# Optimization experiments

Hardware: AMD Instinct MI355X
Metric: run time of the kernel (lower is better)

Reference implementation:

```python
import jax, jax.numpy as jnp
import numpy as np

IN_DIM = 4
H_DIM = 128
OBS_LEN = 15
PRED_LEN = 15
BATCH = 32768


def _lstm_cell(x, h, c, Wih, Whh, bih, bhh):
    # PyTorch gate order: i, f, g, o
    gates = x @ Wih.T + h @ Whh.T + (bih + bhh)  # [B, 4H]
    i, f, g, o = jnp.split(gates, 4, axis=-1)
    c_new = jax.nn.sigmoid(f) * c + jax.nn.sigmoid(i) * jnp.tanh(g)
    h_new = jax.nn.sigmoid(o) * jnp.tanh(c_new)
    return h_new, c_new


def setup_inputs() -> dict:
    key = jax.random.key(0)
    ks = jax.random.split(key, 12)
    s = 1.0 / np.sqrt(H_DIM)  # PyTorch LSTM/Linear uniform init bound
    u = lambda k, shape: jax.random.uniform(k, shape, jnp.float32, -s, s)
    return {
        "x": jax.random.normal(ks[0], (BATCH, OBS_LEN, IN_DIM), jnp.float32),
        "enc_Wih": u(ks[1], (4 * H_DIM, IN_DIM)),
        "enc_Whh": u(ks[2], (4 * H_DIM, H_DIM)),
        "enc_bih": u(ks[3], (4 * H_DIM,)),
        "enc_bhh": u(ks[4], (4 * H_DIM,)),
        "dec_Wih": u(ks[5], (4 * H_DIM, IN_DIM)),
        "dec_Whh": u(ks[6], (4 * H_DIM, H_DIM)),
        "dec_bih": u(ks[7], (4 * H_DIM,)),
        "dec_bhh": u(ks[8], (4 * H_DIM,)),
        "out_W": u(ks[9], (IN_DIM, H_DIM)),
        "out_b": u(ks[10], (IN_DIM,)),
    }


def reference(x, enc_Wih, enc_Whh, enc_bih, enc_bhh,
              dec_Wih, dec_Whh, dec_bih, dec_bhh, out_W, out_b):
    B = x.shape[0]
    h0 = jnp.zeros((B, H_DIM), x.dtype)
    c0 = jnp.zeros((B, H_DIM), x.dtype)

    # ---- encode: run LSTM over time, keep final h ----
    def enc_step(carry, xt):
        h, c = carry
        h, c = _lstm_cell(xt, h, c, enc_Wih, enc_Whh, enc_bih, enc_bhh)
        return (h, c), None

    (h_enc, _), _ = jax.lax.scan(enc_step, (h0, c0), jnp.swapaxes(x, 0, 1))

    def dec_step(carry, _):
        x0, h, c = carry
        h, c = _lstm_cell(x0, h, c, dec_Wih, dec_Whh, dec_bih, dec_bhh)
        x0 = h @ out_W.T + out_b  # [B, IN_DIM]
        return (x0, h, c), x0

    x0 = x[:, -1, :]
    _, preds = jax.lax.scan(dec_step, (x0, h_enc, h_enc), None, length=PRED_LEN)
    return jnp.swapaxes(preds, 0, 1)  # [B, PRED_LEN, IN_DIM]
```

## Files before the change

### kernel.cpp

```cpp
#include <hip/hip_runtime.h>

#define HD   128
#define SEQ  15
#define BN   32
#define LDH  168
#define KT   5
#define NTHR 512

typedef __bf16 bf16x8 __attribute__((ext_vector_type(8)));
typedef unsigned short us8 __attribute__((ext_vector_type(8)));
typedef float f32x4 __attribute__((ext_vector_type(4)));

__device__ __forceinline__ unsigned short f2bf(float f) {
  unsigned int u = __builtin_bit_cast(unsigned int, f);
  u += 0x7fffu + ((u >> 16) & 1u);
  return (unsigned short)(u >> 16);
}
__device__ __forceinline__ float bfl(unsigned int u) {
  return __builtin_bit_cast(float, u << 16);
}
__device__ __forceinline__ float bfh(unsigned int u) {
  return __builtin_bit_cast(float, u & 0xffff0000u);
}
__device__ __forceinline__ float sigm(float v) {
  return __builtin_amdgcn_rcpf(1.0f + __expf(-v));
}
__device__ __forceinline__ float tanh_(float v) {
  return 1.0f - 2.0f * __builtin_amdgcn_rcpf(1.0f + __expf(2.0f * v));
}

__global__ __launch_bounds__(NTHR, 2) void lstm_encdec_kernel(
    const float* __restrict__ x,
    const float* __restrict__ eWih, const float* __restrict__ eWhh,
    const float* __restrict__ ebih, const float* __restrict__ ebhh,
    const float* __restrict__ dWih, const float* __restrict__ dWhh,
    const float* __restrict__ dbih, const float* __restrict__ dbhh,
    const float* __restrict__ oW,  const float* __restrict__ ob,
    float* __restrict__ out)
{
  const int tid  = (int)threadIdx.x;
  const int wv   = tid >> 6;
  const int lane = tid & 63;
  const int l15  = lane & 15;
  const int lk   = lane >> 4;
  const int b0   = (int)blockIdx.x * BN;

  __shared__ alignas(16) unsigned short hbuf[BN][LDH];
  __shared__ float ow_l[4][132];
  __shared__ float ob_l[4];

  bf16x8 bw[4][KT];
  float  bias[4];
  f32x4  cst[2], hst[2];

  for (int i = tid; i < BN * LDH; i += NTHR) ((unsigned short*)hbuf)[i] = 0;

  #pragma unroll
  for (int m = 0; m < 2; ++m)
    #pragma unroll
    for (int j = 0; j < 4; ++j) { cst[m][j] = 0.0f; hst[m][j] = 0.0f; }

  auto load_w = [&](const float* Wih, const float* Whh,
                    const float* bih, const float* bhh, bool fold) {
    #pragma unroll
    for (int g = 0; g < 4; ++g) {
      const int gc = g * HD + wv * 16 + l15;
      float wi[4];
      #pragma unroll
      for (int d = 0; d < 4; ++d) wi[d] = Wih[gc * 4 + d];
      #pragma unroll
      for (int kt = 0; kt < KT; ++kt) {
        const int k0 = kt * 32 + lk * 8;
        float v[8];
        if (k0 < HD) {
          const float4* p = (const float4*)&Whh[(size_t)gc * HD + k0];
          const float4 u0 = p[0], u1 = p[1];
          v[0]=u0.x; v[1]=u0.y; v[2]=u0.z; v[3]=u0.w;
          v[4]=u1.x; v[5]=u1.y; v[6]=u1.z; v[7]=u1.w;
          if (fold) {
            #pragma unroll
            for (int j = 0; j < 8; ++j) {
              float s = v[j];
              #pragma unroll
              for (int d = 0; d < 4; ++d) s += wi[d] * oW[d * HD + k0 + j];
              v[j] = s;
            }
          }
        } else {
          #pragma unroll
          for (int j = 0; j < 8; ++j) {
            v[j] = 0.0f;
            if (j < 4 && lk == 0) v[j] = wi[j];
          }
        }
        us8 u;
        #pragma unroll
        for (int j = 0; j < 8; ++j) u[j] = f2bf(v[j]);
        bw[g][kt] = __builtin_bit_cast(bf16x8, u);
      }
      float bb = bih[gc] + bhh[gc];
      if (fold) {
        #pragma unroll
        for (int d = 0; d < 4; ++d) bb += ob[d] * Wih[gc * 4 + d];
      }
      bias[g] = bb;
    }
  };

  auto mfma_step = [&](f32x4 (&acc)[2][4]) {
    #pragma unroll
    for (int m = 0; m < 2; ++m)
      #pragma unroll
      for (int g = 0; g < 4; ++g)
        #pragma unroll
        for (int j = 0; j < 4; ++j) acc[m][g][j] = bias[g];
    #pragma unroll
    for (int kt = 0; kt < KT; ++kt) {
      #pragma unroll
      for (int m = 0; m < 2; ++m) {
        const bf16x8 a = __builtin_bit_cast(bf16x8,
            *(const uint4*)&hbuf[m * 16 + l15][kt * 32 + lk * 8]);
        #pragma unroll
        for (int g = 0; g < 4; ++g)
          acc[m][g] = __builtin_amdgcn_mfma_f32_16x16x32_bf16(a, bw[g][kt], acc[m][g], 0, 0, 0);
      }
    }
  };

  auto act_update = [&](f32x4 (&acc)[2][4]) {
    #pragma unroll
    for (int m = 0; m < 2; ++m) {
      #pragma unroll
      for (int j = 0; j < 4; ++j) {
        const float iv = sigm(acc[m][0][j]);
        const float fv = sigm(acc[m][1][j]);
        const float gv = tanh_(acc[m][2][j]);
        const float ov = sigm(acc[m][3][j]);
        const float cv = fv * cst[m][j] + iv * gv;
        cst[m][j] = cv;
        hst[m][j] = ov * tanh_(cv);
      }
    }
  };

  auto write_h = [&]() {
    #pragma unroll
    for (int m = 0; m < 2; ++m)
      #pragma unroll
      for (int j = 0; j < 4; ++j)
        hbuf[m * 16 + lk * 4 + j][wv * 16 + l15] = f2bf(hst[m][j]);
  };

  auto proj = [&](int b, int d) {
    float s = ob_l[d];
    #pragma unroll
    for (int k = 0; k < HD; k += 8) {
      const uint4 hv = *(const uint4*)&hbuf[b][k];
      const float* wr = &ow_l[d][k];
      s += bfl(hv.x) * wr[0] + bfh(hv.x) * wr[1]
         + bfl(hv.y) * wr[2] + bfh(hv.y) * wr[3]
         + bfl(hv.z) * wr[4] + bfh(hv.z) * wr[5]
         + bfl(hv.w) * wr[6] + bfh(hv.w) * wr[7];
    }
    return s;
  };

  load_w(eWih, eWhh, ebih, ebhh, false);
  __syncthreads();
  if (tid < BN) {
    const float4 xv = *(const float4*)&x[(size_t)(b0 + tid) * 60];
    *(unsigned int*)&hbuf[tid][HD]     = (unsigned)f2bf(xv.x) | ((unsigned)f2bf(xv.y) << 16);
    *(unsigned int*)&hbuf[tid][HD + 2] = (unsigned)f2bf(xv.z) | ((unsigned)f2bf(xv.w) << 16);
  }
  __syncthreads();

  for (int t = 0; t < SEQ; ++t) {
    f32x4 acc[2][4];
    mfma_step(acc);
    __syncthreads();
    act_update(acc);
    write_h();
    if (t < SEQ - 1 && tid < BN) {
      const float4 xv = *(const float4*)&x[(size_t)(b0 + tid) * 60 + (t + 1) * 4];
      *(unsigned int*)&hbuf[tid][HD]     = (unsigned)f2bf(xv.x) | ((unsigned)f2bf(xv.y) << 16);
      *(unsigned int*)&hbuf[tid][HD + 2] = (unsigned)f2bf(xv.z) | ((unsigned)f2bf(xv.w) << 16);
    }
    __syncthreads();
  }

  cst[0] = hst[0]; cst[1] = hst[1];
  load_w(dWih, dWhh, dbih, dbhh, true);
  for (int i = tid; i < 4 * HD; i += NTHR) ow_l[i >> 7][i & 127] = oW[i];
  if (tid < 4) ob_l[tid] = ob[tid];
  __syncthreads();
  if (tid < 128) {
    const int b = tid >> 2, d = tid & 3;
    const float x0v = proj(b, d);
    const float x14 = x[(size_t)(b0 + b) * 60 + 56 + d];
    hbuf[b][HD + d] = f2bf(x14 - x0v);
  }
  __syncthreads();

  for (int t = 0; t < SEQ; ++t) {
    f32x4 acc[2][4];
    mfma_step(acc);
    __syncthreads();
    act_update(acc);
    write_h();
    if (t == 0 && tid < BN) {
      *(unsigned int*)&hbuf[tid][HD]     = 0u;
      *(unsigned int*)&hbuf[tid][HD + 2] = 0u;
    }
    __syncthreads();
    if (tid < 128) {
      const int b = tid >> 2, d = tid & 3;
      out[(size_t)(b0 + b) * 60 + t * 4 + d] = proj(b, d);
    }
  }
}

extern "C" void kernel_launch(void* const* d_in, const int* in_sizes, int n_in,
                              void* d_out, int out_size, void* d_ws, size_t ws_size,
                              hipStream_t stream) {
  const float* x    = (const float*)d_in[0];
  const float* eWih = (const float*)d_in[1];
  const float* eWhh = (const float*)d_in[2];
  const float* ebih = (const float*)d_in[3];
  const float* ebhh = (const float*)d_in[4];
  const float* dWih = (const float*)d_in[5];
  const float* dWhh = (const float*)d_in[6];
  const float* dbih = (const float*)d_in[7];
  const float* dbhh = (const float*)d_in[8];
  const float* oW   = (const float*)d_in[9];
  const float* ob   = (const float*)d_in[10];

  const int batch = in_sizes[0] / (SEQ * 4);
  dim3 grid(batch / BN), block(NTHR);
  lstm_encdec_kernel<<<grid, block, 0, stream>>>(
      x, eWih, eWhh, ebih, ebhh, dWih, dWhh, dbih, dbhh, oW, ob, (float*)d_out);
}
```

Measured before the change: 461.5 us.

## Double-buffer LSTM hidden state, fold bias into MFMA, stage x and outputs in LDS

The hidden-state LDS buffer is double-buffered so each timestep needs one barrier instead of two. The bias moves into the spare K padding column as a hi/lo bf16 pair multiplied by a constant 1.0 column, which removes the per-gate bias registers and the accumulator initialisation. The input sequence is preloaded once into LDS and outputs are collected in LDS for coalesced float4 stores at the end. The output projection is split across 512 threads with shuffle reductions and overlapped with the next step's MFMAs. The costs are extra LDS usage and slightly different bias rounding.

```diff
diff --git a/kernel.cpp b/kernel.cpp
--- a/kernel.cpp
+++ b/kernel.cpp
@@ -16,18 +16,10 @@
   u += 0x7fffu + ((u >> 16) & 1u);
   return (unsigned short)(u >> 16);
 }
-__device__ __forceinline__ float bfl(unsigned int u) {
-  return __builtin_bit_cast(float, u << 16);
-}
-__device__ __forceinline__ float bfh(unsigned int u) {
-  return __builtin_bit_cast(float, u & 0xffff0000u);
-}
-__device__ __forceinline__ float sigm(float v) {
-  return __builtin_amdgcn_rcpf(1.0f + __expf(-v));
-}
-__device__ __forceinline__ float tanh_(float v) {
-  return 1.0f - 2.0f * __builtin_amdgcn_rcpf(1.0f + __expf(2.0f * v));
-}
+__device__ __forceinline__ float bfl(unsigned int u) { return __builtin_bit_cast(float, u << 16); }
+__device__ __forceinline__ float bfh(unsigned int u) { return __builtin_bit_cast(float, u & 0xffff0000u); }
+__device__ __forceinline__ float sigm(float v) { return __builtin_amdgcn_rcpf(1.0f + __expf(-v)); }
+__device__ __forceinline__ float tanh_(float v) { return 1.0f - 2.0f * __builtin_amdgcn_rcpf(1.0f + __expf(2.0f * v)); }
 
 __global__ __launch_bounds__(NTHR, 2) void lstm_encdec_kernel(
     const float* __restrict__ x,
@@ -45,16 +37,18 @@
   const int lk   = lane >> 4;
   const int b0   = (int)blockIdx.x * BN;
 
-  __shared__ alignas(16) unsigned short hbuf[BN][LDH];
-  __shared__ float ow_l[4][132];
+  const int pv = tid >> 2, pb = pv >> 2, pd = pv & 3, pq = tid & 3;
+
+  __shared__ alignas(16) unsigned short hb[2][BN][LDH];
+  __shared__ alignas(16) unsigned short xbuf[BN][68];
+  __shared__ alignas(16) float obuf[BN][68];
+  __shared__ float ow_l[4][133];
   __shared__ float ob_l[4];
 
   bf16x8 bw[4][KT];
-  float  bias[4];
   f32x4  cst[2], hst[2];
 
-  for (int i = tid; i < BN * LDH; i += NTHR) ((unsigned short*)hbuf)[i] = 0;
-
+  for (int i = tid; i < 2 * BN * LDH; i += NTHR) ((unsigned short*)hb)[i] = 0;
   #pragma unroll
   for (int m = 0; m < 2; ++m)
     #pragma unroll
@@ -68,29 +62,24 @@
       float wi[4];
       #pragma unroll
       for (int d = 0; d < 4; ++d) wi[d] = Wih[gc * 4 + d];
-      #pragma unroll
-      for (int kt = 0; kt < KT; ++kt) {
+      float bb = bih[gc] + bhh[gc];
+      if (fold) {
+        #pragma unroll
+        for (int d = 0; d < 4; ++d) bb += ob[d] * wi[d];
+      }
+      #pragma unroll
+      for (int kt = 0; kt < KT - 1; ++kt) {
         const int k0 = kt * 32 + lk * 8;
-        float v[8];
-        if (k0 < HD) {
-          const float4* p = (const float4*)&Whh[(size_t)gc * HD + k0];
-          const float4 u0 = p[0], u1 = p[1];
-          v[0]=u0.x; v[1]=u0.y; v[2]=u0.z; v[3]=u0.w;
-          v[4]=u1.x; v[5]=u1.y; v[6]=u1.z; v[7]=u1.w;
-          if (fold) {
-            #pragma unroll
-            for (int j = 0; j < 8; ++j) {
-              float s = v[j];
-              #pragma unroll
-              for (int d = 0; d < 4; ++d) s += wi[d] * oW[d * HD + k0 + j];
-              v[j] = s;
-            }
-          }
-        } else {
+        const float4* p = (const float4*)&Whh[(size_t)gc * HD + k0];
+        const float4 u0 = p[0], u1 = p[1];
+        float v[8] = {u0.x, u0.y, u0.z, u0.w, u1.x, u1.y, u1.z, u1.w};
+        if (fold) {
           #pragma unroll
           for (int j = 0; j < 8; ++j) {
-            v[j] = 0.0f;
-            if (j < 4 && lk == 0) v[j] = wi[j];
+            float s = v[j];
+            #pragma unroll
+            for (int d = 0; d < 4; ++d) s += wi[d] * oW[d * HD + k0 + j];
+            v[j] = s;
           }
         }
         us8 u;
@@ -98,28 +87,31 @@
         for (int j = 0; j < 8; ++j) u[j] = f2bf(v[j]);
         bw[g][kt] = __builtin_bit_cast(bf16x8, u);
       }
-      float bb = bih[gc] + bhh[gc];
-      if (fold) {
-        #pragma unroll
-        for (int d = 0; d < 4; ++d) bb += ob[d] * Wih[gc * 4 + d];
-      }
-      bias[g] = bb;
-    }
-  };
-
-  auto mfma_step = [&](f32x4 (&acc)[2][4]) {
+      us8 u4 = {0, 0, 0, 0, 0, 0, 0, 0};
+      if (lk == 0) {
+        #pragma unroll
+        for (int j = 0; j < 4; ++j) u4[j] = f2bf(wi[j]);
+        const unsigned short bh = f2bf(bb);
+        u4[4] = bh;
+        u4[5] = f2bf(bb - bfl((unsigned)bh));
+      }
+      bw[g][KT - 1] = __builtin_bit_cast(bf16x8, u4);
+    }
+  };
+
+  auto mfma_step = [&](f32x4 (&acc)[2][4], int p) {
     #pragma unroll
     for (int m = 0; m < 2; ++m)
       #pragma unroll
       for (int g = 0; g < 4; ++g)
         #pragma unroll
-        for (int j = 0; j < 4; ++j) acc[m][g][j] = bias[g];
+        for (int j = 0; j < 4; ++j) acc[m][g][j] = 0.0f;
     #pragma unroll
     for (int kt = 0; kt < KT; ++kt) {
       #pragma unroll
       for (int m = 0; m < 2; ++m) {
         const bf16x8 a = __builtin_bit_cast(bf16x8,
-            *(const uint4*)&hbuf[m * 16 + l15][kt * 32 + lk * 8]);
+            *(const uint4*)&hb[p][m * 16 + l15][kt * 32 + lk * 8]);
         #pragma unroll
         for (int g = 0; g < 4; ++g)
           acc[m][g] = __builtin_amdgcn_mfma_f32_16x16x32_bf16(a, bw[g][kt], acc[m][g], 0, 0, 0);
@@ -129,7 +121,7 @@
 
   auto act_update = [&](f32x4 (&acc)[2][4]) {
     #pragma unroll
-    for (int m = 0; m < 2; ++m) {
+    for (int m = 0; m < 2; ++m)
       #pragma unroll
       for (int j = 0; j < 4; ++j) {
         const float iv = sigm(acc[m][0][j]);
@@ -140,52 +132,65 @@
         cst[m][j] = cv;
         hst[m][j] = ov * tanh_(cv);
       }
-    }
-  };
-
-  auto write_h = [&]() {
+  };
+
+  auto write_h = [&](int pw) {
     #pragma unroll
     for (int m = 0; m < 2; ++m)
       #pragma unroll
       for (int j = 0; j < 4; ++j)
-        hbuf[m * 16 + lk * 4 + j][wv * 16 + l15] = f2bf(hst[m][j]);
-  };
-
-  auto proj = [&](int b, int d) {
-    float s = ob_l[d];
-    #pragma unroll
-    for (int k = 0; k < HD; k += 8) {
-      const uint4 hv = *(const uint4*)&hbuf[b][k];
-      const float* wr = &ow_l[d][k];
-      s += bfl(hv.x) * wr[0] + bfh(hv.x) * wr[1]
-         + bfl(hv.y) * wr[2] + bfh(hv.y) * wr[3]
-         + bfl(hv.z) * wr[4] + bfh(hv.z) * wr[5]
-         + bfl(hv.w) * wr[6] + bfh(hv.w) * wr[7];
-    }
-    return s;
+        hb[pw][m * 16 + lk * 4 + j][wv * 16 + l15] = f2bf(hst[m][j]);
+  };
+
+  auto proj = [&](int p) {
+    float s = 0.0f;
+    #pragma unroll
+    for (int c = 0; c < 4; ++c) {
+      const int rc = (c + pq) & 3;
+      const int k  = pq * 32 + rc * 8;
+      const uint4 hv = *(const uint4*)&hb[p][pb][k];
+      const float* w = &ow_l[pd][k];
+      s += bfl(hv.x) * w[0] + bfh(hv.x) * w[1]
+         + bfl(hv.y) * w[2] + bfh(hv.y) * w[3]
+         + bfl(hv.z) * w[4] + bfh(hv.z) * w[5]
+         + bfl(hv.w) * w[6] + bfh(hv.w) * w[7];
+    }
+    s += __shfl_xor(s, 1);
+    s += __shfl_xor(s, 2);
+    return s + ob_l[pd];
   };
 
   load_w(eWih, eWhh, ebih, ebhh, false);
-  __syncthreads();
+  if (tid < 480) {
+    const int b = tid / 15, c = tid % 15;
+    const float4 xv = *(const float4*)&x[(size_t)(b0 + b) * 60 + c * 4];
+    *(unsigned int*)&xbuf[b][c * 4]     = (unsigned)f2bf(xv.x) | ((unsigned)f2bf(xv.y) << 16);
+    *(unsigned int*)&xbuf[b][c * 4 + 2] = (unsigned)f2bf(xv.z) | ((unsigned)f2bf(xv.w) << 16);
+  }
+  __syncthreads();
+  if (tid < 64) {
+    const int buf = tid >> 5, b = tid & 31;
+    *(unsigned int*)&hb[buf][b][132] = 0x3F803F80u;
+  }
   if (tid < BN) {
-    const float4 xv = *(const float4*)&x[(size_t)(b0 + tid) * 60];
-    *(unsigned int*)&hbuf[tid][HD]     = (unsigned)f2bf(xv.x) | ((unsigned)f2bf(xv.y) << 16);
-    *(unsigned int*)&hbuf[tid][HD + 2] = (unsigned)f2bf(xv.z) | ((unsigned)f2bf(xv.w) << 16);
-  }
-  __syncthreads();
-
+    const uint2 xv = *(const uint2*)&xbuf[tid][0];
+    *(uint2*)&hb[0][tid][128] = xv;
+  }
+  __syncthreads();
+
+  int p = 0;
+  #pragma unroll 2
   for (int t = 0; t < SEQ; ++t) {
     f32x4 acc[2][4];
-    mfma_step(acc);
+    mfma_step(acc, p);
+    act_update(acc);
+    write_h(p ^ 1);
+    if (t < SEQ - 1 && tid < BN) {
+      const uint2 xv = *(const uint2*)&xbuf[tid][(t + 1) * 4];
+      *(uint2*)&hb[p ^ 1][tid][128] = xv;
+    }
     __syncthreads();
-    act_update(acc);
-    write_h();
-    if (t < SEQ - 1 && tid < BN) {
-      const float4 xv = *(const float4*)&x[(size_t)(b0 + tid) * 60 + (t + 1) * 4];
-      *(unsigned int*)&hbuf[tid][HD]     = (unsigned)f2bf(xv.x) | ((unsigned)f2bf(xv.y) << 16);
-      *(unsigned int*)&hbuf[tid][HD + 2] = (unsigned)f2bf(xv.z) | ((unsigned)f2bf(xv.w) << 16);
-    }
-    __syncthreads();
+    p ^= 1;
   }
 
   cst[0] = hst[0]; cst[1] = hst[1];
@@ -193,29 +198,40 @@
   for (int i = tid; i < 4 * HD; i += NTHR) ow_l[i >> 7][i & 127] = oW[i];
   if (tid < 4) ob_l[tid] = ob[tid];
   __syncthreads();
-  if (tid < 128) {
-    const int b = tid >> 2, d = tid & 3;
-    const float x0v = proj(b, d);
-    const float x14 = x[(size_t)(b0 + b) * 60 + 56 + d];
-    hbuf[b][HD + d] = f2bf(x14 - x0v);
-  }
-  __syncthreads();
-
+  {
+    const float s = proj(p);
+    if (pq == 0) {
+      const float x14 = bfl((unsigned)xbuf[pb][56 + pd]);
+      hb[p][pb][128 + pd] = f2bf(x14 - s);
+    }
+  }
+  __syncthreads();
+
+  #pragma unroll 2
   for (int t = 0; t < SEQ; ++t) {
     f32x4 acc[2][4];
-    mfma_step(acc);
+    mfma_step(acc, p);
+    if (t > 0) {
+      const float pr = proj(p);
+      if (pq == 0) obuf[pb][(t - 1) * 4 + pd] = pr;
+    }
+    act_update(acc);
+    write_h(p ^ 1);
+    if (tid < BN)
+      *(uint2*)&hb[p ^ 1][tid][128] = (uint2){0u, 0u};
     __syncthreads();
-    act_update(acc);
-    write_h();
-    if (t == 0 && tid < BN) {
-      *(unsigned int*)&hbuf[tid][HD]     = 0u;
-      *(unsigned int*)&hbuf[tid][HD + 2] = 0u;
-    }
-    __syncthreads();
-    if (tid < 128) {
-      const int b = tid >> 2, d = tid & 3;
-      out[(size_t)(b0 + b) * 60 + t * 4 + d] = proj(b, d);
-    }
+    p ^= 1;
+  }
+  {
+    const float pr = proj(p);
+    if (pq == 0) obuf[pb][14 * 4 + pd] = pr;
+  }
+  __syncthreads();
+
+  if (tid < 480) {
+    const int b = tid / 15, c = tid % 15;
+    const float4 v = *(const float4*)&obuf[b][c * 4];
+    *(float4*)&out[(size_t)(b0 + b) * 60 + c * 4] = v;
   }
 }
 
```

Result: faster. 436.5 us (-5.4%).
